# Performance work log

Hardware: AMD Instinct MI355X
Metric: run time of the kernel (lower is better)

The kernel has to match this reference:

```python
import jax, jax.numpy as jnp
import numpy as np
from jax import lax

B, C, H, W = 8, 256, 64, 64
NUM_HEADS = 4
HEAD_DIM = C // NUM_HEADS  # == dim // 4, required by q_proj
EPS_LN = 1e-5
EPS_NORM = 1e-12


def _gelu(x):
    return jax.nn.gelu(x, approximate=False)  # torch default GELU is erf-based


def setup_inputs() -> dict:
    key = jax.random.key(0)
    ks = jax.random.split(key, 20)
    s = lambda fan_in: 1.0 / np.sqrt(fan_in)
    return {
        "x": jax.random.normal(ks[0], (B, C, H, W), jnp.float32),
        # LayerNorm(dim)
        "ln_g": jnp.ones((C,), jnp.float32),
        "ln_b": jnp.zeros((C,), jnp.float32),
        # qkv: Linear(C, 3C, bias=False); stored (in, out)
        "w_qkv": jax.random.normal(ks[1], (C, 3 * C), jnp.float32) * s(C),
        # q_proj: Linear(head_dim, head_dim); stored (in, out)
        "w_q": jax.random.normal(ks[2], (HEAD_DIM, HEAD_DIM), jnp.float32) * s(HEAD_DIM),
        "b_q": jax.random.normal(ks[3], (HEAD_DIM,), jnp.float32) * 0.01,
        "temperature": jnp.ones((NUM_HEADS, 1, 1), jnp.float32),
        # depthwise 3x3 conv, groups=C: kernel (C,1,3,3) OIHW
        "dw_w": jax.random.normal(ks[4], (C, 1, 3, 3), jnp.float32) * s(9),
        "dw_b": jax.random.normal(ks[5], (C,), jnp.float32) * 0.01,
        # channel_interaction: 1x1 convs stored as (out, in)
        "ci_w1": jax.random.normal(ks[6], (C // 8, C), jnp.float32) * s(C),
        "ci_b1": jax.random.normal(ks[7], (C // 8,), jnp.float32) * 0.01,
        "ci_w2": jax.random.normal(ks[8], (C, C // 8), jnp.float32) * s(C // 8),
        "ci_b2": jax.random.normal(ks[9], (C,), jnp.float32) * 0.01,
        # spatial_interaction: 1x1 convs stored as (out, in)
        "si_w1": jax.random.normal(ks[10], (C // 16, C), jnp.float32) * s(C),
        "si_b1": jax.random.normal(ks[11], (C // 16,), jnp.float32) * 0.01,
        "si_w2": jax.random.normal(ks[12], (1, C // 16), jnp.float32) * s(C // 16),
        "si_b2": jax.random.normal(ks[13], (1,), jnp.float32) * 0.01,
        # proj: Linear(C, C); stored (in, out)
        "proj_w": jax.random.normal(ks[14], (C, C), jnp.float32) * s(C),
        "proj_b": jax.random.normal(ks[15], (C,), jnp.float32) * 0.01,
    }


def reference(x, ln_g, ln_b, w_qkv, w_q, b_q, temperature, dw_w, dw_b,
              ci_w1, ci_b1, ci_w2, ci_b2, si_w1, si_b1, si_w2, si_b2,
              proj_w, proj_b):
    Bx, Cx, Hx, Wx = x.shape
    N = Hx * Wx
    nh = temperature.shape[0]
    hd = Cx // nh

    # before_RG: (B,C,H,W) -> (B,N,C), LayerNorm over C
    xt = x.reshape(Bx, Cx, N).transpose(0, 2, 1)
    mu = xt.mean(-1, keepdims=True)
    var = ((xt - mu) ** 2).mean(-1, keepdims=True)
    xn = (xt - mu) * lax.rsqrt(var + EPS_LN) * ln_g + ln_b

    # qkv -> (3, B, nh, N, hd)
    qkv = (xn @ w_qkv).reshape(Bx, N, 3, nh, hd).transpose(2, 0, 3, 1, 4)
    q, k, v = qkv[0], qkv[1], qkv[2]
    q = q @ w_q + b_q                      # Linear on head_dim
    q = q.transpose(0, 1, 3, 2)            # (B, nh, hd, N)
    k = k.transpose(0, 1, 3, 2)
    v = v.transpose(0, 1, 3, 2)
    v_ = v.reshape(Bx, Cx, Hx, Wx)         # head-major channel layout

    # L2 normalize along N (torch F.normalize semantics)
    q = q / jnp.clip(jnp.linalg.norm(q, axis=-1, keepdims=True), EPS_NORM)
    k = k / jnp.clip(jnp.linalg.norm(k, axis=-1, keepdims=True), EPS_NORM)

    # channel attention: (B, nh, hd, hd)
    attn = jnp.einsum('bhdn,bhen->bhde', q, k) * temperature
    attn = jax.nn.softmax(attn, axis=-1)
    attened_x = jnp.einsum('bhde,bhen->bhdn', attn, v)
    attened_x = attened_x.transpose(0, 3, 1, 2).reshape(Bx, N, Cx)  # (B,N,C)

    # depthwise conv branch + GELU
    conv_x = lax.conv_general_dilated(
        v_, dw_w, window_strides=(1, 1), padding='SAME',
        feature_group_count=Cx, dimension_numbers=('NCHW', 'OIHW', 'NCHW'))
    conv_x = _gelu(conv_x + dw_b[None, :, None, None])

    # channel interaction (SE on attention branch)
    pooled = attened_x.mean(axis=1)                    # (B,C) == global avg pool of (B,C,H,W)
    ci = _gelu(pooled @ ci_w1.T + ci_b1)
    channel_map = ci @ ci_w2.T + ci_b2                 # (B,C)

    # spatial interaction (on conv branch)
    si = _gelu(jnp.einsum('bchw,oc->bohw', conv_x, si_w1) + si_b1[None, :, None, None])
    spatial_map = jnp.einsum('bchw,oc->bohw', si, si_w2) + si_b2[None, :, None, None]  # (B,1,H,W)
    spatial_map = spatial_map.reshape(Bx, N, 1)

    # cross gating and fuse
    attened_x = attened_x * jax.nn.sigmoid(spatial_map)
    conv_x = conv_x * jax.nn.sigmoid(channel_map)[:, :, None, None]
    conv_x = conv_x.reshape(Bx, Cx, N).transpose(0, 2, 1)

    out = (attened_x + conv_x) @ proj_w + proj_b       # (B,N,C)
    return out.transpose(0, 2, 1).reshape(Bx, Cx, Hx, Wx)
```

## Files before the change

kernel.cpp:

```cpp
#include <hip/hip_runtime.h>

typedef unsigned short u16;
typedef short bf16x8 __attribute__((ext_vector_type(8)));
typedef float f32x4 __attribute__((ext_vector_type(4)));

__device__ __forceinline__ float bf2f(u16 u){ return __uint_as_float(((unsigned)u)<<16); }
__device__ __forceinline__ u16 f2bf(float f){
  unsigned u = __float_as_uint(f);
  u += 0x7FFF + ((u >> 16) & 1);
  return (u16)(u >> 16);
}
__device__ __forceinline__ float ldp(const void* p, size_t i, int bf){
  return bf ? bf2f(((const u16*)p)[i]) : ((const float*)p)[i];
}
__device__ __forceinline__ float gelu_f(float x){ return 0.5f*x*(1.0f+erff(x*0.70710678118654752440f)); }
__device__ __forceinline__ float sigmoid_f(float x){ return 1.0f/(1.0f+expf(-x)); }
__device__ __forceinline__ int bfdet(const void* g){ return ((const unsigned*)g)[0] == 0x3F803F80u; }

struct __align__(8)  U16x4 { u16 x,y,z,w; };
struct __align__(16) U16x8 { u16 v[8]; };

#define Cc 256
#define Nn 4096
#define CN 1048576


__global__ __launch_bounds__(256) void k_phase1(const void* __restrict__ x,
                    const void* __restrict__ g, const void* __restrict__ bta,
                    const void* __restrict__ wqkv, const void* __restrict__ wq,
                    const void* __restrict__ bq, const void* __restrict__ pw,
                    u16* __restrict__ xn16,
                    u16* __restrict__ WallT16, u16* __restrict__ pwT16,
                    float* __restrict__ biasall, float* __restrict__ zbase){
  __shared__ float tile[256*65];
  __shared__ float gs[256], bs[256];
  __shared__ float red_s[4][64], red_ss[4][64];
  __shared__ float mu_sh[64], rs_sh[64];
  int tid = threadIdx.x;
  int bid = blockIdx.x;
  int bf = bfdet(g);
  if (bid >= 512){
    int j = bid - 512;
    int c = tid;
    if (j >= 1024){
      size_t i = (size_t)(j - 1024)*1024 + c*4;
      float4 z; z.x=0.f; z.y=0.f; z.z=0.f; z.w=0.f;
      *(float4*)(zbase + i) = z;
      return;
    }
    if (j < 768){
      float out;
      if (j < 256){
        int h = j >> 6, e = j & 63;
        float acc = 0.f;
        #pragma unroll 8
        for (int d = 0; d < 64; ++d)
          acc += ldp(wqkv, c*768 + h*64 + d, bf) * ldp(wq, d*64 + e, bf);
        out = acc;
      } else {
        out = ldp(wqkv, c*768 + j, bf);
      }
      size_t a = ((size_t)((j>>4)*8 + (c>>5))*64 + (j&15) + 16*((c>>3)&3))*8 + (c&7);
      WallT16[a] = f2bf(out);
      if (c == 0) biasall[j] = (j < 256) ? ldp(bq, j & 63, bf) : 0.f;
    } else {
      int o = j - 768;
      size_t a = ((size_t)((o>>4)*8 + (c>>5))*64 + (o&15) + 16*((c>>3)&3))*8 + (c&7);
      pwT16[a] = f2bf(ldp(pw, c*256 + o, bf));
    }
    return;
  }
  int b  = bid >> 6;
  int n0 = (bid & 63) * 64;
  gs[tid] = ldp(g, tid, bf); bs[tid] = ldp(bta, tid, bf);
  int crow = tid >> 2, noff = (tid & 3) * 16;
  for (int p = 0; p < 4; ++p){
    int c = p*64 + crow;
    size_t base = (size_t)b*CN + (size_t)c*Nn + n0 + noff;
    float vals[16];
    if (bf){
      #pragma unroll
      for (int q = 0; q < 2; ++q){
        U16x8 u = *(const U16x8*)((const u16*)x + base + q*8);
        #pragma unroll
        for (int i = 0; i < 8; ++i) vals[q*8+i] = bf2f(u.v[i]);
      }
    } else {
      #pragma unroll
      for (int q = 0; q < 4; ++q){
        float4 f = *(const float4*)((const float*)x + base + q*4);
        vals[q*4+0]=f.x; vals[q*4+1]=f.y; vals[q*4+2]=f.z; vals[q*4+3]=f.w;
      }
    }
    #pragma unroll
    for (int i = 0; i < 16; ++i) tile[c*65 + noff + i] = vals[i];
  }
  __syncthreads();
  {
    int r = tid >> 6, nl = tid & 63;
    float s = 0.f, ss = 0.f;
    for (int cc = r*64; cc < r*64 + 64; ++cc){
      float v = tile[cc*65 + nl];
      s += v; ss += v*v;
    }
    red_s[r][nl] = s; red_ss[r][nl] = ss;
  }
  __syncthreads();
  if (tid < 64){
    float st  = red_s[0][tid]  + red_s[1][tid]  + red_s[2][tid]  + red_s[3][tid];
    float sst = red_ss[0][tid] + red_ss[1][tid] + red_ss[2][tid] + red_ss[3][tid];
    float m   = st * (1.f/256.f);
    float var = sst * (1.f/256.f) - m*m;
    mu_sh[tid] = m;
    rs_sh[tid] = rsqrtf(var + 1e-5f);
  }
  __syncthreads();
  int n = tid >> 2, coff = (tid & 3) * 64;
  float mn = mu_sh[n], rn = rs_sh[n];
  int gidx = (n0 >> 4) + (n >> 4);
  int l15 = n & 15;
  u16* dstb = xn16 + ((size_t)b*256 + gidx)*4096;
  for (int q = 0; q < 8; ++q){
    int c8 = coff + q*8;
    int ks = c8 >> 5, quad = (c8 >> 3) & 3;
    U16x8 w;
    #pragma unroll
    for (int i = 0; i < 8; ++i){
      int c = c8 + i;
      w.v[i] = f2bf((tile[c*65 + n] - mn)*rn*gs[c] + bs[c]);
    }
    *(U16x8*)(dstb + (size_t)ks*512 + (l15 + 16*quad)*8) = w;
  }
}

__global__ __launch_bounds__(256, 4) void k_qkv(const u16* __restrict__ xn16,
                                             const u16* __restrict__ WallT16,
                                             const float* __restrict__ biasall,
                                             u16* __restrict__ q16, u16* __restrict__ k16,
                                             u16* __restrict__ v16, u16* __restrict__ vT16,
                                             float* __restrict__ qsq, float* __restrict__ ksq){
  __shared__ u16 Bs[16384];
  __shared__ float bias_sh[64];
  __shared__ float sq_sh[64];
  int tid = threadIdx.x;
  int by = blockIdx.x;
  int bx = blockIdx.y;
  int b  = by >> 5;
  int n0 = (by & 31) * 128;
  int j0 = bx * 64;
  int part = bx >> 2;
  int h = (j0 >> 6) & 3;
  int w = tid >> 6, lane = tid & 63, l15 = lane & 15, quad = lane >> 4;

  const u16* Afrag = xn16 + ((size_t)b*256 + (n0>>4) + w*2)*4096 + lane*8;
  bf16x8 af[2][8];
  #pragma unroll
  for (int r = 0; r < 2; ++r)
    #pragma unroll
    for (int ks = 0; ks < 8; ++ks)
      af[r][ks] = *(const bf16x8*)(Afrag + (size_t)r*4096 + (size_t)ks*512);

  const u16* Bt = WallT16 + (size_t)(j0>>4)*4096;
  #pragma unroll
  for (int i = 0; i < 8; ++i){
    int off = (i*256 + tid)*8;
    *(bf16x8*)(Bs + off) = *(const bf16x8*)(Bt + off);
  }
  if (tid < 64){ bias_sh[tid] = biasall[j0 + tid]; sq_sh[tid] = 0.f; }
  __syncthreads();

  f32x4 acc[2][4];
  #pragma unroll
  for (int r=0;r<2;++r)
    #pragma unroll
    for (int s=0;s<4;++s){ acc[r][s][0]=0.f; acc[r][s][1]=0.f; acc[r][s][2]=0.f; acc[r][s][3]=0.f; }

  const u16* Bfrag = Bs + lane*8;
  #pragma unroll
  for (int ks = 0; ks < 8; ++ks){
    #pragma unroll
    for (int s = 0; s < 4; ++s){
      bf16x8 bb = *(const bf16x8*)(Bfrag + s*4096 + ks*512);
      acc[0][s] = __builtin_amdgcn_mfma_f32_16x16x32_bf16(af[0][ks], bb, acc[0][s], 0, 0, 0);
      acc[1][s] = __builtin_amdgcn_mfma_f32_16x16x32_bf16(af[1][ks], bb, acc[1][s], 0, 0, 0);
    }
  }
  u16* dst = (part==0) ? q16 : ((part==1) ? k16 : v16);
  float sql[4];
  #pragma unroll
  for (int s=0;s<4;++s) sql[s]=0.f;
  #pragma unroll
  for (int r = 0; r < 2; ++r){
    int nb = n0 + w*32 + r*16 + quad*4;
    #pragma unroll
    for (int s = 0; s < 4; ++s){
      int d = s*16 + l15;
      float bd = bias_sh[d];
      float v0 = acc[r][s][0] + bd, v1 = acc[r][s][1] + bd;
      float v2 = acc[r][s][2] + bd, v3 = acc[r][s][3] + bd;
      U16x4 wv; wv.x=f2bf(v0); wv.y=f2bf(v1); wv.z=f2bf(v2); wv.w=f2bf(v3);
      *(U16x4*)(dst + ((size_t)(b*4 + h)*64 + d)*4096 + nb) = wv;
      sql[s] += v0*v0 + v1*v1 + v2*v2 + v3*v3;
    }
  }
  if (part < 2){
    #pragma unroll
    for (int s = 0; s < 4; ++s)
      atomicAdd(&sq_sh[s*16 + l15], sql[s]);
    __syncthreads();
    if (tid < 64){
      float* nsq = (part==0) ? qsq : ksq;
      atomicAdd(&nsq[(b*4 + h)*64 + tid], sq_sh[tid]);
    }
  } else {
    __syncthreads();
    u16* Ls = Bs;
    #pragma unroll
    for (int r = 0; r < 2; ++r){
      #pragma unroll
      for (int s = 0; s < 4; ++s){
        int d = s*16 + l15;
        #pragma unroll
        for (int i = 0; i < 4; ++i){
          int nl = w*32 + r*16 + quad*4 + i;
          Ls[nl*72 + d] = f2bf(acc[r][s][i]);
        }
      }
    }
    __syncthreads();
    u16* vt = vT16 + ((size_t)(b*4 + h))*262144 + (size_t)(n0>>4)*1024;
    #pragma unroll
    for (int it = 0; it < 4; ++it){
      int lin = it*256 + tid;
      int t15 = lin & 15, q4 = (lin>>4)&3, ks = (lin>>6)&1, g = lin>>7;
      int nl = g*16 + t15;
      int e0 = ks*32 + q4*8;
      U16x8 wv = *(const U16x8*)&Ls[nl*72 + e0];
      *(U16x8*)(vt + (size_t)lin*8) = wv;
    }
  }
}

__global__ __launch_bounds__(256) void k_phase3(const u16* __restrict__ q16,
                                                const u16* __restrict__ k16,
                                                float* __restrict__ S,
                                                const u16* __restrict__ v16,
                                                const void* __restrict__ dww,
                                                const void* __restrict__ dwb,
                                                const unsigned* __restrict__ g_bits,
                                                u16* __restrict__ conv16){
  __shared__ float plane[4096];
  int tid = threadIdx.x;
  int bid = blockIdx.x;
  if (bid < 512){
    int bh = bid >> 4;
    int kc = bid & 15;
    int w = tid >> 6, lane = tid & 63, l15 = lane & 15, quad = lane >> 4;
    f32x4 acc[4];
    #pragma unroll
    for (int s=0;s<4;++s){ acc[s][0]=0.f; acc[s][1]=0.f; acc[s][2]=0.f; acc[s][3]=0.f; }
    const u16* qp = q16 + ((size_t)bh*64 + w*16 + l15)*4096 + quad*8;
    const u16* kp = k16 + ((size_t)bh*64 + l15)*4096 + quad*8;
    #pragma unroll 4
    for (int nn = kc*256; nn < kc*256 + 256; nn += 32){
      bf16x8 a = *(const bf16x8*)(qp + nn);
      #pragma unroll
      for (int s = 0; s < 4; ++s){
        bf16x8 bb = *(const bf16x8*)(kp + (size_t)s*16*4096 + nn);
        acc[s] = __builtin_amdgcn_mfma_f32_16x16x32_bf16(a, bb, acc[s], 0, 0, 0);
      }
    }
    float* Sb = S + (size_t)bh*4096;
    #pragma unroll
    for (int s = 0; s < 4; ++s)
      #pragma unroll
      for (int i = 0; i < 4; ++i)
        atomicAdd(&Sb[(w*16 + quad*4 + i)*64 + s*16 + l15], acc[s][i]);
    return;
  }
  int bf = bfdet(g_bits);
  int bc = bid - 512;
  int c = bc & 255;
  const u16* vp = v16 + (size_t)bc*4096;
  #pragma unroll
  for (int i = 0; i < 4; ++i){
    int lin = (i*256 + tid)*4;
    U16x4 vu = *(const U16x4*)(vp + lin);
    plane[lin+0]=bf2f(vu.x); plane[lin+1]=bf2f(vu.y); plane[lin+2]=bf2f(vu.z); plane[lin+3]=bf2f(vu.w);
  }
  float wgt[9];
  #pragma unroll
  for (int i = 0; i < 9; ++i) wgt[i] = ldp(dww, c*9 + i, bf);
  float bias = ldp(dwb, c, bf);
  __syncthreads();
  int y = tid >> 2, x0 = (tid & 3) * 16;
  float r[3][18];
  #pragma unroll
  for (int ky = 0; ky < 3; ++ky){
    int yy = y + ky - 1;
    if (yy < 0 || yy > 63){
      #pragma unroll
      for (int j = 0; j < 18; ++j) r[ky][j] = 0.f;
    } else {
      const float* rp = &plane[yy*64 + x0];
      r[ky][0]  = (x0 == 0)  ? 0.f : rp[-1];
      r[ky][17] = (x0 == 48) ? 0.f : rp[16];
      #pragma unroll
      for (int q = 0; q < 4; ++q){
        float4 f = *(const float4*)(rp + q*4);
        r[ky][1+q*4+0]=f.x; r[ky][1+q*4+1]=f.y; r[ky][1+q*4+2]=f.z; r[ky][1+q*4+3]=f.w;
      }
    }
  }
  U16x8 o0, o1;
  #pragma unroll
  for (int x = 0; x < 16; ++x){
    float acc = bias;
    #pragma unroll
    for (int ky = 0; ky < 3; ++ky)
      #pragma unroll
      for (int kx = 0; kx < 3; ++kx)
        acc += wgt[ky*3+kx] * r[ky][x+kx];
    u16 ov = f2bf(gelu_f(acc));
    if (x < 8) o0.v[x] = ov; else o1.v[x-8] = ov;
  }
  u16* op = conv16 + (size_t)bc*4096 + y*64 + x0;
  *(U16x8*)op = o0;
  *(U16x8*)(op + 8) = o1;
}

__global__ __launch_bounds__(256) void k_phase4(const float* __restrict__ S,
                                                const float* __restrict__ qsq,
                                                const float* __restrict__ ksq,
                                                const void* __restrict__ temp,
                                                const unsigned* __restrict__ g_bits,
                                                const u16* __restrict__ vT16,
                                                u16* __restrict__ attT,
                                                float* __restrict__ pooled,
                                                const u16* __restrict__ conv16,
                                                const void* __restrict__ w1, const void* __restrict__ b1,
                                                const void* __restrict__ w2, const void* __restrict__ b2,
                                                float* __restrict__ ssp){
  __shared__ __align__(16) unsigned char smem[41984];
  int tid = threadIdx.x;
  int bid = blockIdx.x;
  int bf = bfdet(g_bits);
  if (bid < 512){
    u16*   Bs   = (u16*)smem;
    u16*   P_sh = (u16*)(smem + 32768);
    float* kn   = (float*)(smem + 40960);
    float* qn   = (float*)(smem + 41216);
    float* red  = (float*)(smem + 41472);
    int bh = bid >> 4;
    int n0 = (bid & 15) * 256;
    int w = tid >> 6, lane = tid & 63, l15 = lane & 15, quad = lane >> 4;
    int b = bh >> 2, h = bh & 3;
    if (tid < 64){
      kn[tid] = fmaxf(sqrtf(ksq[bh*64 + tid]), 1e-12f);
      qn[tid] = fmaxf(sqrtf(qsq[bh*64 + tid]), 1e-12f);
      red[tid] = 0.f;
    }
    const u16* vt = vT16 + (size_t)bh*262144 + (size_t)(n0>>4)*1024;
    #pragma unroll
    for (int i = 0; i < 8; ++i){
      int off = (i*256 + tid)*8;
      *(bf16x8*)(Bs + off) = *(const bf16x8*)(vt + off);
    }
    __syncthreads();
    {
      int d  = tid >> 2;
      int e0 = (tid & 3) * 16;
      float tpr = ldp(temp, h, bf);
      const float* row = S + (size_t)bh*4096 + d*64 + e0;
      float sc = tpr / qn[d];
      float v[16];
      #pragma unroll
      for (int q = 0; q < 4; ++q){
        float4 f = *(const float4*)(row + q*4);
        v[q*4+0]=f.x; v[q*4+1]=f.y; v[q*4+2]=f.z; v[q*4+3]=f.w;
      }
      float mx = -1e30f;
      #pragma unroll
      for (int e = 0; e < 16; ++e){
        v[e] = v[e] * sc / kn[e0 + e];
        mx = fmaxf(mx, v[e]);
      }
      mx = fmaxf(mx, __shfl_xor(mx, 1));
      mx = fmaxf(mx, __shfl_xor(mx, 2));
      float s = 0.f;
      #pragma unroll
      for (int e = 0; e < 16; ++e){ v[e] = expf(v[e] - mx); s += v[e]; }
      s += __shfl_xor(s, 1);
      s += __shfl_xor(s, 2);
      float inv = 1.f/s;
      int g = d >> 4, l15d = d & 15;
      #pragma unroll
      for (int half = 0; half < 2; ++half){
        int e = e0 + half*8;
        int ks = e >> 5, q4 = (e >> 3) & 3;
        U16x8 wv;
        #pragma unroll
        for (int i = 0; i < 8; ++i) wv.v[i] = f2bf(v[half*8 + i]*inv);
        *(U16x8*)(P_sh + ((g*2 + ks)*64 + l15d + 16*q4)*8) = wv;
      }
    }
    __syncthreads();
    bf16x8 af0 = *(const bf16x8*)(P_sh + ((w*2 + 0)*64 + lane)*8);
    bf16x8 af1 = *(const bf16x8*)(P_sh + ((w*2 + 1)*64 + lane)*8);
    f32x4 acc[16];
    #pragma unroll
    for (int s = 0; s < 16; ++s){ acc[s][0]=0.f; acc[s][1]=0.f; acc[s][2]=0.f; acc[s][3]=0.f; }
    const u16* Bfrag = Bs + lane*8;
    #pragma unroll
    for (int s = 0; s < 16; ++s){
      bf16x8 b0 = *(const bf16x8*)(Bfrag + (s*2 + 0)*512);
      bf16x8 b1 = *(const bf16x8*)(Bfrag + (s*2 + 1)*512);
      acc[s] = __builtin_amdgcn_mfma_f32_16x16x32_bf16(af0, b0, acc[s], 0, 0, 0);
      acc[s] = __builtin_amdgcn_mfma_f32_16x16x32_bf16(af1, b1, acc[s], 0, 0, 0);
    }
    u16* ob = attT + ((size_t)b*4096 + n0)*256 + h*64 + w*16 + quad*4;
    float p0=0.f, p1=0.f, p2=0.f, p3=0.f;
    #pragma unroll
    for (int s = 0; s < 16; ++s){
      int n = s*16 + l15;
      U16x4 wv; wv.x=f2bf(acc[s][0]); wv.y=f2bf(acc[s][1]); wv.z=f2bf(acc[s][2]); wv.w=f2bf(acc[s][3]);
      *(U16x4*)(ob + (size_t)n*256) = wv;
      p0 += acc[s][0]; p1 += acc[s][1]; p2 += acc[s][2]; p3 += acc[s][3];
    }
    atomicAdd(&red[w*16 + quad*4 + 0], p0);
    atomicAdd(&red[w*16 + quad*4 + 1], p1);
    atomicAdd(&red[w*16 + quad*4 + 2], p2);
    atomicAdd(&red[w*16 + quad*4 + 3], p3);
    __syncthreads();
    if (tid < 64)
      atomicAdd(&pooled[b*256 + h*64 + tid], red[tid]);
    return;
  }
  {
    float* w1s = (float*)smem;
    u16*   tl  = (u16*)(smem + 16448);
    int idx = bid - 512;
    int b  = idx >> 7;
    int n0 = (idx & 127) * 32;
    #pragma unroll
    for (int i = 0; i < 16; ++i)
      w1s[i*257 + tid] = ldp(w1, i*256 + tid, bf);
    const u16* cb = conv16 + (size_t)b*CN + n0;
    #pragma unroll
    for (int i = 0; i < 4; ++i){
      int id2 = i*256 + tid;
      int c = id2 >> 2, seg = id2 & 3;
      *(U16x8*)&tl[c*40 + seg*8] = *(const U16x8*)(cb + (size_t)c*Nn + seg*8);
    }
    __syncthreads();
    int og = tid & 7, nl = tid >> 3;
    int o = og*2;
    float a0 = 0.f, a1 = 0.f;
    #pragma unroll 8
    for (int cc = 0; cc < 256; ++cc){
      float xv = bf2f(tl[cc*40 + nl]);
      a0 += xv * w1s[o*257 + cc];
      a1 += xv * w1s[(o+1)*257 + cc];
    }
    float sp = gelu_f(a0 + ldp(b1, o, bf)) * ldp(w2, o, bf)
             + gelu_f(a1 + ldp(b1, o+1, bf)) * ldp(w2, o+1, bf);
    sp += __shfl_xor(sp, 1);
    sp += __shfl_xor(sp, 2);
    sp += __shfl_xor(sp, 4);
    if (og == 0)
      ssp[(size_t)b*Nn + n0 + nl] = sigmoid_f(sp + ldp(b2, 0, bf));
  }
}

__global__ __launch_bounds__(512) void k_phase5(const u16* __restrict__ attT,
                                             const u16* __restrict__ conv16,
                                             const float* __restrict__ ssp,
                                             const float* __restrict__ pooled,
                                             const void* __restrict__ cw1, const void* __restrict__ cb1,
                                             const void* __restrict__ cw2, const void* __restrict__ cb2,
                                             const u16* __restrict__ pwT16,
                                             const void* __restrict__ pb,
                                             const unsigned* __restrict__ g_bits,
                                             void* __restrict__ out){
  __shared__ u16 ct[256*72];
  __shared__ u16 at[64*264];
  __shared__ u16 Yf[32768];
  __shared__ float ssp_sh[64], sch_sh[256], pb_sh[256];
  __shared__ float ps[256], cis[32];
  int bf = bfdet(g_bits);
  int tid = threadIdx.x;
  int b  = blockIdx.x >> 6;
  int n0 = (blockIdx.x & 63) * 64;
  int w2 = tid >> 6, lane = tid & 63, l15 = lane & 15, quad = lane >> 4;
  int mg = w2 & 3, chalf = w2 >> 2;

  if (tid < 256){ ps[tid] = pooled[b*256 + tid] * (1.f/4096.f); pb_sh[tid] = ldp(pb, tid, bf); }
  if (tid < 64) ssp_sh[tid] = ssp[(size_t)b*Nn + n0 + tid];
  const u16* cb = conv16 + (size_t)b*CN + n0;
  #pragma unroll
  for (int i = 0; i < 4; ++i){
    int idx = i*512 + tid;
    int c = idx >> 3, seg = idx & 7;
    *(U16x8*)&ct[c*72 + seg*8] = *(const U16x8*)(cb + (size_t)c*Nn + seg*8);
  }
  const u16* ab = attT + ((size_t)b*4096 + n0)*256;
  #pragma unroll
  for (int i = 0; i < 4; ++i){
    int idx = i*512 + tid;
    int n = idx >> 5, seg = idx & 31;
    *(U16x8*)&at[n*264 + seg*8] = *(const U16x8*)(ab + (size_t)n*256 + seg*8);
  }
  __syncthreads();
  if (tid < 32){
    float a = ldp(cb1, tid, bf);
    #pragma unroll 8
    for (int cc = 0; cc < 256; ++cc) a += ps[cc]*ldp(cw1, tid*256 + cc, bf);
    cis[tid] = gelu_f(a);
  }
  __syncthreads();
  if (tid < 256){
    float m = ldp(cb2, tid, bf);
    #pragma unroll
    for (int o = 0; o < 32; ++o) m += cis[o]*ldp(cw2, tid*32 + o, bf);
    sch_sh[tid] = sigmoid_f(m);
  }
  __syncthreads();
  #pragma unroll
  for (int it = 0; it < 4; ++it){
    int lin = it*512 + tid;
    int tl15 = lin & 15, q4 = (lin>>4)&3, ks = (lin>>6)&7, ng = lin>>9;
    int n = ng*16 + tl15;
    int c0 = ks*32 + q4*8;
    float gn = ssp_sh[n];
    U16x8 av = *(const U16x8*)&at[n*264 + c0];
    U16x8 wv;
    #pragma unroll
    for (int i = 0; i < 8; ++i){
      int c = c0 + i;
      wv.v[i] = f2bf(bf2f(av.v[i])*gn + bf2f(ct[c*72 + n])*sch_sh[c]);
    }
    *(U16x8*)(Yf + (size_t)lin*8) = wv;
  }
  __syncthreads();
  bf16x8 af[8];
  #pragma unroll
  for (int ks = 0; ks < 8; ++ks)
    af[ks] = *(const bf16x8*)(Yf + ((size_t)(mg*8 + ks)*64 + lane)*8);
  f32x4 acc[8];
  #pragma unroll
  for (int s=0;s<8;++s){ acc[s][0]=0.f; acc[s][1]=0.f; acc[s][2]=0.f; acc[s][3]=0.f; }
  #pragma unroll
  for (int sl = 0; sl < 8; ++sl){
    int s = chalf*8 + sl;
    #pragma unroll
    for (int ks = 0; ks < 8; ++ks){
      bf16x8 bb = *(const bf16x8*)(pwT16 + ((size_t)(s*8 + ks))*512 + lane*8);
      acc[sl] = __builtin_amdgcn_mfma_f32_16x16x32_bf16(af[ks], bb, acc[sl], 0, 0, 0);
    }
  }
  int nbase = n0 + mg*16 + quad*4;
  #pragma unroll
  for (int sl = 0; sl < 8; ++sl){
    int cout = chalf*128 + sl*16 + l15;
    float pbias = pb_sh[cout];
    size_t oidx = ((size_t)(b*256 + cout))*4096 + nbase;
    float v0 = acc[sl][0] + pbias, v1 = acc[sl][1] + pbias;
    float v2 = acc[sl][2] + pbias, v3 = acc[sl][3] + pbias;
    if (bf){
      U16x4 wv; wv.x=f2bf(v0); wv.y=f2bf(v1); wv.z=f2bf(v2); wv.w=f2bf(v3);
      *(U16x4*)((u16*)out + oidx) = wv;
    } else {
      float4 wv; wv.x=v0; wv.y=v1; wv.z=v2; wv.w=v3;
      *(float4*)((float*)out + oidx) = wv;
    }
  }
}

extern "C" void kernel_launch(void* const* d_in, const int* in_sizes, int n_in,
                              void* d_out, int out_size, void* d_ws, size_t ws_size,
                              hipStream_t stream) {
  const void* x    = d_in[0];
  const void* ln_g = d_in[1];
  const void* ln_b = d_in[2];
  const void* wqkv = d_in[3];
  const void* wq   = d_in[4];
  const void* bq   = d_in[5];
  const void* temp = d_in[6];
  const void* dww  = d_in[7];
  const void* dwb  = d_in[8];
  const void* ciw1 = d_in[9];
  const void* cib1 = d_in[10];
  const void* ciw2 = d_in[11];
  const void* cib2 = d_in[12];
  const void* siw1 = d_in[13];
  const void* sib1 = d_in[14];
  const void* siw2 = d_in[15];
  const void* sib2 = d_in[16];
  const void* pw   = d_in[17];
  const void* pb   = d_in[18];

  u16* wsu    = (u16*)d_ws;
  u16* q16    = wsu;
  u16* k16    = wsu + 8388608;
  u16* xn16   = wsu + 16777216;
  u16* attT   = q16;
  u16* conv16 = xn16;
  u16* v16    = (u16*)d_out;

  u16* vT16;
  if (out_size >= 33554432) vT16 = (u16*)d_out + 8388608;
  else                      vT16 = wsu + 25165824;

  float* tail = (float*)(wsu + 33554432);
  float* qsq  = tail;
  float* ksq  = qsq + 2048;
  float* S    = ksq + 2048;
  float* pool = S + 131072;
  float* biasall = pool + 2048;
  float* ssp  = biasall + 768;
  u16* WallT16 = (u16*)(ssp + 32768);
  u16* pwT16   = WallT16 + 196608;

  hipLaunchKernelGGL(k_phase1, dim3(1670), dim3(256), 0, stream,
                     x, ln_g, ln_b, wqkv, wq, bq, pw, xn16, WallT16, pwT16, biasall, qsq);
  hipLaunchKernelGGL(k_qkv,    dim3(256, 12), dim3(256), 0, stream,
                     xn16, WallT16, biasall, q16, k16, v16, vT16, qsq, ksq);
  hipLaunchKernelGGL(k_phase3, dim3(2560), dim3(256), 0, stream,
                     q16, k16, S, v16, dww, dwb, (const unsigned*)ln_g, conv16);
  hipLaunchKernelGGL(k_phase4, dim3(1536), dim3(256), 0, stream,
                     S, qsq, ksq, temp, (const unsigned*)ln_g, vT16, attT, pool,
                     conv16, siw1, sib1, siw2, sib2, ssp);
  hipLaunchKernelGGL(k_phase5, dim3(512), dim3(512), 0, stream,
                     attT, conv16, ssp, pool, ciw1, cib1, ciw2, cib2,
                     pwT16, pb, (const unsigned*)ln_g, d_out);
}
```

Baseline: 297.8 us.

## Halve phase5 tile to 32 positions, transpose conv tile, build MFMA operands in registers

The final projection kernel now handles 32 spatial positions per block instead of 64, which doubles the grid and cuts shared memory roughly in half (the Yf staging buffer is removed). The conv tile is stored transposed so each lane can read its gated A-fragment directly from LDS, and the extra staging pass and barrier go away. The channel-interaction MLP's first layer is parallelised across all 512 threads with shuffle reductions, replacing 32 serial threads. The risks are that per-block SE recomputation is duplicated across twice as many blocks, and the scalar transposed LDS writes may cause bank conflicts.

```diff
diff --git a/kernel.cpp b/kernel.cpp
--- a/kernel.cpp
+++ b/kernel.cpp
@@ -482,40 +482,47 @@
                                              const void* __restrict__ pb,
                                              const unsigned* __restrict__ g_bits,
                                              void* __restrict__ out){
-  __shared__ u16 ct[256*72];
-  __shared__ u16 at[64*264];
-  __shared__ u16 Yf[32768];
-  __shared__ float ssp_sh[64], sch_sh[256], pb_sh[256];
-  __shared__ float ps[256], cis[32];
+  __shared__ u16 ctT[32*264];
+  __shared__ u16 at[32*264];
+  __shared__ float ssp_sh[32], sch_sh[256], pb_sh[256], ps[256], cis[32];
   int bf = bfdet(g_bits);
   int tid = threadIdx.x;
-  int b  = blockIdx.x >> 6;
-  int n0 = (blockIdx.x & 63) * 64;
+  int b  = blockIdx.x >> 7;
+  int n0 = (blockIdx.x & 127) * 32;
   int w2 = tid >> 6, lane = tid & 63, l15 = lane & 15, quad = lane >> 4;
-  int mg = w2 & 3, chalf = w2 >> 2;
+  int mg = w2 & 1, cq = w2 >> 1;
 
   if (tid < 256){ ps[tid] = pooled[b*256 + tid] * (1.f/4096.f); pb_sh[tid] = ldp(pb, tid, bf); }
-  if (tid < 64) ssp_sh[tid] = ssp[(size_t)b*Nn + n0 + tid];
+  if (tid < 32) ssp_sh[tid] = ssp[(size_t)b*Nn + n0 + tid];
   const u16* cb = conv16 + (size_t)b*CN + n0;
   #pragma unroll
-  for (int i = 0; i < 4; ++i){
+  for (int i = 0; i < 2; ++i){
     int idx = i*512 + tid;
-    int c = idx >> 3, seg = idx & 7;
-    *(U16x8*)&ct[c*72 + seg*8] = *(const U16x8*)(cb + (size_t)c*Nn + seg*8);
+    int c = idx >> 2, seg = idx & 3;
+    U16x8 u = *(const U16x8*)(cb + (size_t)c*Nn + seg*8);
+    #pragma unroll
+    for (int t = 0; t < 8; ++t)
+      ctT[(seg*8 + t)*264 + c] = u.v[t];
   }
   const u16* ab = attT + ((size_t)b*4096 + n0)*256;
   #pragma unroll
-  for (int i = 0; i < 4; ++i){
+  for (int i = 0; i < 2; ++i){
     int idx = i*512 + tid;
     int n = idx >> 5, seg = idx & 31;
     *(U16x8*)&at[n*264 + seg*8] = *(const U16x8*)(ab + (size_t)n*256 + seg*8);
   }
   __syncthreads();
-  if (tid < 32){
-    float a = ldp(cb1, tid, bf);
-    #pragma unroll 8
-    for (int cc = 0; cc < 256; ++cc) a += ps[cc]*ldp(cw1, tid*256 + cc, bf);
-    cis[tid] = gelu_f(a);
+  {
+    int o = tid >> 4, sub = tid & 15;
+    float a = 0.f;
+    #pragma unroll
+    for (int q = 0; q < 16; ++q){
+      int cc = sub*16 + q;
+      a += ps[cc] * ldp(cw1, o*256 + cc, bf);
+    }
+    a += __shfl_xor(a, 1); a += __shfl_xor(a, 2);
+    a += __shfl_xor(a, 4); a += __shfl_xor(a, 8);
+    if (sub == 0) cis[o] = gelu_f(a + ldp(cb1, o, bf));
   }
   __syncthreads();
   if (tid < 256){
@@ -525,43 +532,36 @@
     sch_sh[tid] = sigmoid_f(m);
   }
   __syncthreads();
-  #pragma unroll
-  for (int it = 0; it < 4; ++it){
-    int lin = it*512 + tid;
-    int tl15 = lin & 15, q4 = (lin>>4)&3, ks = (lin>>6)&7, ng = lin>>9;
-    int n = ng*16 + tl15;
-    int c0 = ks*32 + q4*8;
-    float gn = ssp_sh[n];
+  int n = mg*16 + l15;
+  float gn = ssp_sh[n];
+  bf16x8 af[8];
+  #pragma unroll
+  for (int ks = 0; ks < 8; ++ks){
+    int c0 = ks*32 + quad*8;
     U16x8 av = *(const U16x8*)&at[n*264 + c0];
+    U16x8 cv = *(const U16x8*)&ctT[n*264 + c0];
     U16x8 wv;
     #pragma unroll
-    for (int i = 0; i < 8; ++i){
-      int c = c0 + i;
-      wv.v[i] = f2bf(bf2f(av.v[i])*gn + bf2f(ct[c*72 + n])*sch_sh[c]);
-    }
-    *(U16x8*)(Yf + (size_t)lin*8) = wv;
-  }
-  __syncthreads();
-  bf16x8 af[8];
-  #pragma unroll
-  for (int ks = 0; ks < 8; ++ks)
-    af[ks] = *(const bf16x8*)(Yf + ((size_t)(mg*8 + ks)*64 + lane)*8);
-  f32x4 acc[8];
-  #pragma unroll
-  for (int s=0;s<8;++s){ acc[s][0]=0.f; acc[s][1]=0.f; acc[s][2]=0.f; acc[s][3]=0.f; }
-  #pragma unroll
-  for (int sl = 0; sl < 8; ++sl){
-    int s = chalf*8 + sl;
+    for (int t = 0; t < 8; ++t)
+      wv.v[t] = f2bf(bf2f(av.v[t])*gn + bf2f(cv.v[t])*sch_sh[c0 + t]);
+    af[ks] = *(bf16x8*)&wv;
+  }
+  f32x4 acc[4];
+  #pragma unroll
+  for (int s=0;s<4;++s){ acc[s][0]=0.f; acc[s][1]=0.f; acc[s][2]=0.f; acc[s][3]=0.f; }
+  #pragma unroll
+  for (int sl = 0; sl < 4; ++sl){
+    int gout = cq*4 + sl;
     #pragma unroll
     for (int ks = 0; ks < 8; ++ks){
-      bf16x8 bb = *(const bf16x8*)(pwT16 + ((size_t)(s*8 + ks))*512 + lane*8);
+      bf16x8 bb = *(const bf16x8*)(pwT16 + ((size_t)(gout*8 + ks))*512 + lane*8);
       acc[sl] = __builtin_amdgcn_mfma_f32_16x16x32_bf16(af[ks], bb, acc[sl], 0, 0, 0);
     }
   }
   int nbase = n0 + mg*16 + quad*4;
   #pragma unroll
-  for (int sl = 0; sl < 8; ++sl){
-    int cout = chalf*128 + sl*16 + l15;
+  for (int sl = 0; sl < 4; ++sl){
+    int cout = cq*64 + sl*16 + l15;
     float pbias = pb_sh[cout];
     size_t oidx = ((size_t)(b*256 + cout))*4096 + nbase;
     float v0 = acc[sl][0] + pbias, v1 = acc[sl][1] + pbias;
@@ -630,7 +630,7 @@
   hipLaunchKernelGGL(k_phase4, dim3(1536), dim3(256), 0, stream,
                      S, qsq, ksq, temp, (const unsigned*)ln_g, vT16, attT, pool,
                      conv16, siw1, sib1, siw2, sib2, ssp);
-  hipLaunchKernelGGL(k_phase5, dim3(512), dim3(512), 0, stream,
+  hipLaunchKernelGGL(k_phase5, dim3(1024), dim3(512), 0, stream,
                      attT, conv16, ssp, pool, ciw1, cib1, ciw2, cib2,
                      pwT16, pb, (const unsigned*)ln_g, d_out);
 }
```

Result: faster. 284.6 us (-4.4%).

## Split final phase into channel-SE, gating, and tiled projection kernels

Applied to the files above, without the earlier changes.

Replaces the monolithic phase-5 kernel with three kernels. The channel-interaction MLP now runs once per batch instead of being recomputed in every block. The gated sum is written to a global bf16 buffer in MFMA fragment order, and a separate projection GEMM kernel with a 2D grid of 1024 blocks keeps a 64-column weight tile in LDS. The goal is to remove redundant SE work and raise occupancy of the projection. The cost is an extra global write and read of the gated tensor plus two extra launches.

```diff
diff --git a/kernel.cpp b/kernel.cpp
--- a/kernel.cpp
+++ b/kernel.cpp
@@ -472,64 +472,63 @@
   }
 }
 
-__global__ __launch_bounds__(512) void k_phase5(const u16* __restrict__ attT,
-                                             const u16* __restrict__ conv16,
-                                             const float* __restrict__ ssp,
-                                             const float* __restrict__ pooled,
-                                             const void* __restrict__ cw1, const void* __restrict__ cb1,
-                                             const void* __restrict__ cw2, const void* __restrict__ cb2,
-                                             const u16* __restrict__ pwT16,
-                                             const void* __restrict__ pb,
-                                             const unsigned* __restrict__ g_bits,
-                                             void* __restrict__ out){
-  __shared__ u16 ct[256*72];
+__global__ void k_channel(const float* __restrict__ pooled,
+                          const void* __restrict__ w1, const void* __restrict__ b1,
+                          const void* __restrict__ w2, const void* __restrict__ b2,
+                          const unsigned* __restrict__ g_bits,
+                          float* __restrict__ sch){
+  __shared__ float ps[256];
+  __shared__ float cis[32];
+  int bf = bfdet(g_bits);
+  int b = blockIdx.x, tid = threadIdx.x;
+  ps[tid] = pooled[b*256 + tid] * (1.f/4096.f);
+  __syncthreads();
+  if (tid < 32){
+    float a = ldp(b1, tid, bf);
+    for (int cc = 0; cc < 256; ++cc) a += ps[cc]*ldp(w1, tid*256 + cc, bf);
+    cis[tid] = gelu_f(a);
+  }
+  __syncthreads();
+  float m = ldp(b2, tid, bf);
+  #pragma unroll
+  for (int o = 0; o < 32; ++o) m += cis[o]*ldp(w2, tid*32 + o, bf);
+  sch[b*256 + tid] = sigmoid_f(m);
+}
+
+__global__ __launch_bounds__(256) void k_gate(const u16* __restrict__ attT,
+                                              const u16* __restrict__ conv16,
+                                              const float* __restrict__ ssp,
+                                              const float* __restrict__ sch,
+                                              u16* __restrict__ Y16){
+  __shared__ u16 ct[256*66];
   __shared__ u16 at[64*264];
-  __shared__ u16 Yf[32768];
-  __shared__ float ssp_sh[64], sch_sh[256], pb_sh[256];
-  __shared__ float ps[256], cis[32];
-  int bf = bfdet(g_bits);
+  __shared__ float ssp_sh[64], sch_sh[256];
   int tid = threadIdx.x;
   int b  = blockIdx.x >> 6;
   int n0 = (blockIdx.x & 63) * 64;
-  int w2 = tid >> 6, lane = tid & 63, l15 = lane & 15, quad = lane >> 4;
-  int mg = w2 & 3, chalf = w2 >> 2;
-
-  if (tid < 256){ ps[tid] = pooled[b*256 + tid] * (1.f/4096.f); pb_sh[tid] = ldp(pb, tid, bf); }
+  sch_sh[tid] = sch[b*256 + tid];
   if (tid < 64) ssp_sh[tid] = ssp[(size_t)b*Nn + n0 + tid];
   const u16* cb = conv16 + (size_t)b*CN + n0;
   #pragma unroll
-  for (int i = 0; i < 4; ++i){
-    int idx = i*512 + tid;
+  for (int i = 0; i < 8; ++i){
+    int idx = i*256 + tid;
     int c = idx >> 3, seg = idx & 7;
-    *(U16x8*)&ct[c*72 + seg*8] = *(const U16x8*)(cb + (size_t)c*Nn + seg*8);
+    *(U16x8*)&ct[c*66 + seg*8] = *(const U16x8*)(cb + (size_t)c*Nn + seg*8);
   }
   const u16* ab = attT + ((size_t)b*4096 + n0)*256;
   #pragma unroll
-  for (int i = 0; i < 4; ++i){
-    int idx = i*512 + tid;
+  for (int i = 0; i < 8; ++i){
+    int idx = i*256 + tid;
     int n = idx >> 5, seg = idx & 31;
     *(U16x8*)&at[n*264 + seg*8] = *(const U16x8*)(ab + (size_t)n*256 + seg*8);
   }
   __syncthreads();
-  if (tid < 32){
-    float a = ldp(cb1, tid, bf);
-    #pragma unroll 8
-    for (int cc = 0; cc < 256; ++cc) a += ps[cc]*ldp(cw1, tid*256 + cc, bf);
-    cis[tid] = gelu_f(a);
-  }
-  __syncthreads();
-  if (tid < 256){
-    float m = ldp(cb2, tid, bf);
-    #pragma unroll
-    for (int o = 0; o < 32; ++o) m += cis[o]*ldp(cw2, tid*32 + o, bf);
-    sch_sh[tid] = sigmoid_f(m);
-  }
-  __syncthreads();
-  #pragma unroll
-  for (int it = 0; it < 4; ++it){
-    int lin = it*512 + tid;
-    int tl15 = lin & 15, q4 = (lin>>4)&3, ks = (lin>>6)&7, ng = lin>>9;
-    int n = ng*16 + tl15;
+  u16* dstb = Y16 + ((size_t)b*256 + (n0>>4))*4096;
+  #pragma unroll
+  for (int it = 0; it < 8; ++it){
+    int lin = it*256 + tid;
+    int l15 = lin & 15, q4 = (lin>>4)&3, ks = (lin>>6)&7, ng = lin>>9;
+    int n = ng*16 + l15;
     int c0 = ks*32 + q4*8;
     float gn = ssp_sh[n];
     U16x8 av = *(const U16x8*)&at[n*264 + c0];
@@ -537,41 +536,78 @@
     #pragma unroll
     for (int i = 0; i < 8; ++i){
       int c = c0 + i;
-      wv.v[i] = f2bf(bf2f(av.v[i])*gn + bf2f(ct[c*72 + n])*sch_sh[c]);
-    }
-    *(U16x8*)(Yf + (size_t)lin*8) = wv;
-  }
-  __syncthreads();
-  bf16x8 af[8];
-  #pragma unroll
-  for (int ks = 0; ks < 8; ++ks)
-    af[ks] = *(const bf16x8*)(Yf + ((size_t)(mg*8 + ks)*64 + lane)*8);
-  f32x4 acc[8];
-  #pragma unroll
-  for (int s=0;s<8;++s){ acc[s][0]=0.f; acc[s][1]=0.f; acc[s][2]=0.f; acc[s][3]=0.f; }
-  #pragma unroll
-  for (int sl = 0; sl < 8; ++sl){
-    int s = chalf*8 + sl;
-    #pragma unroll
-    for (int ks = 0; ks < 8; ++ks){
-      bf16x8 bb = *(const bf16x8*)(pwT16 + ((size_t)(s*8 + ks))*512 + lane*8);
-      acc[sl] = __builtin_amdgcn_mfma_f32_16x16x32_bf16(af[ks], bb, acc[sl], 0, 0, 0);
-    }
-  }
-  int nbase = n0 + mg*16 + quad*4;
-  #pragma unroll
-  for (int sl = 0; sl < 8; ++sl){
-    int cout = chalf*128 + sl*16 + l15;
-    float pbias = pb_sh[cout];
-    size_t oidx = ((size_t)(b*256 + cout))*4096 + nbase;
-    float v0 = acc[sl][0] + pbias, v1 = acc[sl][1] + pbias;
-    float v2 = acc[sl][2] + pbias, v3 = acc[sl][3] + pbias;
-    if (bf){
-      U16x4 wv; wv.x=f2bf(v0); wv.y=f2bf(v1); wv.z=f2bf(v2); wv.w=f2bf(v3);
-      *(U16x4*)((u16*)out + oidx) = wv;
-    } else {
-      float4 wv; wv.x=v0; wv.y=v1; wv.z=v2; wv.w=v3;
-      *(float4*)((float*)out + oidx) = wv;
+      wv.v[i] = f2bf(bf2f(av.v[i])*gn + bf2f(ct[c*66 + n])*sch_sh[c]);
+    }
+    *(U16x8*)(dstb + (size_t)lin*8) = wv;
+  }
+}
+
+__global__ __launch_bounds__(256, 4) void k_proj(const u16* __restrict__ Y16,
+                                              const u16* __restrict__ pwT16,
+                                              const void* __restrict__ pb,
+                                              const unsigned* __restrict__ g_bits,
+                                              void* __restrict__ out){
+  __shared__ u16 Bs[16384];
+  __shared__ float pb_sh[64];
+  int bf = bfdet(g_bits);
+  int tid = threadIdx.x;
+  int by = blockIdx.x;
+  int bx = blockIdx.y;
+  int b  = by >> 5;
+  int n0 = (by & 31) * 128;
+  int c0 = bx * 64;
+  int w = tid >> 6, lane = tid & 63, l15 = lane & 15, quad = lane >> 4;
+
+  const u16* Afrag = Y16 + ((size_t)b*256 + (n0>>4) + w*2)*4096 + lane*8;
+  bf16x8 af[2][8];
+  #pragma unroll
+  for (int r = 0; r < 2; ++r)
+    #pragma unroll
+    for (int ks = 0; ks < 8; ++ks)
+      af[r][ks] = *(const bf16x8*)(Afrag + (size_t)r*4096 + (size_t)ks*512);
+
+  const u16* Bt = pwT16 + (size_t)(c0>>4)*4096;
+  #pragma unroll
+  for (int i = 0; i < 8; ++i){
+    int off = (i*256 + tid)*8;
+    *(bf16x8*)(Bs + off) = *(const bf16x8*)(Bt + off);
+  }
+  if (tid < 64) pb_sh[tid] = ldp(pb, c0 + tid, bf);
+  __syncthreads();
+
+  f32x4 acc[2][4];
+  #pragma unroll
+  for (int r=0;r<2;++r)
+    #pragma unroll
+    for (int s=0;s<4;++s){ acc[r][s][0]=0.f; acc[r][s][1]=0.f; acc[r][s][2]=0.f; acc[r][s][3]=0.f; }
+
+  const u16* Bfrag = Bs + lane*8;
+  #pragma unroll
+  for (int ks = 0; ks < 8; ++ks){
+    #pragma unroll
+    for (int s = 0; s < 4; ++s){
+      bf16x8 bb = *(const bf16x8*)(Bfrag + s*4096 + ks*512);
+      acc[0][s] = __builtin_amdgcn_mfma_f32_16x16x32_bf16(af[0][ks], bb, acc[0][s], 0, 0, 0);
+      acc[1][s] = __builtin_amdgcn_mfma_f32_16x16x32_bf16(af[1][ks], bb, acc[1][s], 0, 0, 0);
+    }
+  }
+  #pragma unroll
+  for (int r = 0; r < 2; ++r){
+    int nb = n0 + w*32 + r*16 + quad*4;
+    #pragma unroll
+    for (int s = 0; s < 4; ++s){
+      int cch = c0 + s*16 + l15;
+      float pbias = pb_sh[s*16 + l15];
+      size_t oidx = ((size_t)(b*256 + cch))*4096 + nb;
+      float v0 = acc[r][s][0] + pbias, v1 = acc[r][s][1] + pbias;
+      float v2 = acc[r][s][2] + pbias, v3 = acc[r][s][3] + pbias;
+      if (bf){
+        U16x4 wv; wv.x=f2bf(v0); wv.y=f2bf(v1); wv.z=f2bf(v2); wv.w=f2bf(v3);
+        *(U16x4*)((u16*)out + oidx) = wv;
+      } else {
+        float4 wv; wv.x=v0; wv.y=v1; wv.z=v2; wv.w=v3;
+        *(float4*)((float*)out + oidx) = wv;
+      }
     }
   }
 }
@@ -605,6 +641,7 @@
   u16* xn16   = wsu + 16777216;
   u16* attT   = q16;
   u16* conv16 = xn16;
+  u16* Y16    = k16;
   u16* v16    = (u16*)d_out;
 
   u16* vT16;
@@ -617,7 +654,8 @@
   float* S    = ksq + 2048;
   float* pool = S + 131072;
   float* biasall = pool + 2048;
-  float* ssp  = biasall + 768;
+  float* sch  = biasall + 768;
+  float* ssp  = sch + 2048;
   u16* WallT16 = (u16*)(ssp + 32768);
   u16* pwT16   = WallT16 + 196608;
 
@@ -630,7 +668,10 @@
   hipLaunchKernelGGL(k_phase4, dim3(1536), dim3(256), 0, stream,
                      S, qsq, ksq, temp, (const unsigned*)ln_g, vT16, attT, pool,
                      conv16, siw1, sib1, siw2, sib2, ssp);
-  hipLaunchKernelGGL(k_phase5, dim3(512), dim3(512), 0, stream,
-                     attT, conv16, ssp, pool, ciw1, cib1, ciw2, cib2,
-                     pwT16, pb, (const unsigned*)ln_g, d_out);
-}
+  hipLaunchKernelGGL(k_channel, dim3(8), dim3(256), 0, stream,
+                     pool, ciw1, cib1, ciw2, cib2, (const unsigned*)ln_g, sch);
+  hipLaunchKernelGGL(k_gate,   dim3(512), dim3(256), 0, stream,
+                     attT, conv16, ssp, sch, Y16);
+  hipLaunchKernelGGL(k_proj,   dim3(256, 4), dim3(256), 0, stream,
+                     Y16, pwT16, pb, (const unsigned*)ln_g, d_out);
+}
```

After: 278.0 us. -6.7%, faster.
